# Kernel tuning notes

Hardware: AMD Instinct MI355X
Metric: run time of the kernel (lower is better)

## Reference

```python
import jax, jax.numpy as jnp
import numpy as np

KERNEL_SIZE = 5
SIGMA = 1.0
CHANNELS = 13
MAX_LEVELS = 3


def gaussian_kernel(size=KERNEL_SIZE, channels=CHANNELS, sigma=SIGMA):
    ax = np.linspace(-(size - 1) / 2.0, (size - 1) / 2.0, size)
    xx, yy = np.meshgrid(ax, ax)
    k = np.exp(-0.5 * (np.square(xx) + np.square(yy)) / np.square(sigma))
    k /= np.sum(k)
    # depthwise OIHW: (channels, 1, kh, kw), same kernel per channel
    return jnp.asarray(np.tile(k[None, None], (channels, 1, 1, 1)), dtype=jnp.float32)


def depthwise_gauss(x, kernel):
    c = kernel.shape[0]
    pad = kernel.shape[-1] // 2
    return jax.lax.conv_general_dilated(
        x, kernel, window_strides=(1, 1),
        padding=[(pad, pad), (pad, pad)],
        dimension_numbers=('NCHW', 'OIHW', 'NCHW'),
        feature_group_count=c)


def downsample(x):
    return x[:, :, ::2, ::2]


def upsample_nearest2x(x):
    return jnp.repeat(jnp.repeat(x, 2, axis=2), 2, axis=3)


def create_laplacian_pyramid(x, kernel, levels):
    pyramids = []
    cur = x
    for _ in range(levels):
        down = downsample(depthwise_gauss(cur, kernel))
        pyramids.append(cur - upsample_nearest2x(down))
        cur = down
    pyramids.append(cur)
    return pyramids


def setup_inputs() -> dict:
    key = jax.random.key(0)
    k1, k2 = jax.random.split(key)
    B, C, H, W = 16, CHANNELS, 512, 512
    x = jax.random.normal(k1, (B, C, H, W), dtype=jnp.float32)
    target = jax.random.normal(k2, (B, C, H, W), dtype=jnp.float32)
    kernel = gaussian_kernel()  # deterministic buffer, matches torch module
    return {"x": x, "target": target, "kernel": kernel}


def reference(x, target, kernel):
    x = x.astype(jnp.float32)
    target = target.astype(jnp.float32)
    px = create_laplacian_pyramid(x, kernel, MAX_LEVELS)
    pt = create_laplacian_pyramid(target, kernel, MAX_LEVELS)
    # torch F.l1_loss default reduction='mean' per level, summed over levels
    loss = jnp.asarray(0.0, dtype=jnp.float32)
    for a, b in zip(px, pt):
        loss = loss + jnp.mean(jnp.abs(a - b))
    return loss
```

## Files before the change

kernel.cpp:

```cpp
#include <hip/hip_runtime.h>


constexpr int THREADS = 256;
constexpr int TC = 32, TR = 16;
constexpr int ROWS = 2*TR + 3;
constexpr int COLS = 2*TC + 8;
constexpr int SEG4 = COLS/4;
constexpr int TOT4 = ROWS*SEG4;
constexpr int WOPS = (TOT4 + 63)/64;
constexpr int WREG = WOPS*64*4;
constexpr int HR = 11;

__device__ inline void gload_lds16(const float* g, float* l) {
    auto g1 = (const __attribute__((address_space(1))) void*)g;
    auto l3 = (__attribute__((address_space(3))) void*)l;
    __builtin_amdgcn_global_load_lds(g1, l3, 16, 0, 0);
}

template <int MW, bool FUSE, bool LAST, bool WRITE_DOWN>
__global__ __launch_bounds__(THREADS, MW)
void lap_level(const float* __restrict__ A,
               const float* __restrict__ Bp,
               const float* __restrict__ w25,
               float* __restrict__ down,
               float* __restrict__ P,
               int H, int W, int ntx, int nty, int ntiles, int level)
{
    __shared__ __align__(16) float sdA[2][WREG];
    __shared__ __align__(16) float sdB[2][FUSE ? WREG : 4];
    __shared__ float sdH[4][HR*TC];
    __shared__ float wsl[4], wsd[4];

    const int tid  = threadIdx.x;
    const int wv   = tid >> 6, lane = tid & 63;
    const int Hd = H >> 1, Wd = W >> 1;
    const int ntxy = ntx * nty;

    float g0, g1, g2, g3, g4;
    {
        float gg[5];
#pragma unroll
        for (int i = 0; i < 5; ++i) {
            float s = 0.f;
#pragma unroll
            for (int j = 0; j < 5; ++j) s += w25[i*5 + j];
            gg[i] = s;
        }
        g0 = gg[0]; g1 = gg[1]; g2 = gg[2]; g3 = gg[3]; g4 = gg[4];
    }

    float lsum = 0.f, dsum = 0.f;
    int cur = blockIdx.x;

    auto stage = [&](int t, int pp) {
        const int n   = t / ntxy;
        const int rem = t - n*ntxy;
        const int ty  = rem / ntx;
        const int tx  = rem - ty*ntx;
        const int gy0 = 2*ty*TR - 2;
        const int gx0 = 2*tx*TC - 4;
        const size_t ib = (size_t)n * H * W;
        for (int j = wv; j < WOPS; j += 4) {
            const int idx4 = j*64 + lane;
            const int r  = idx4 / SEG4;
            const int c4 = idx4 - r*SEG4;
            int gy = gy0 + r;          gy = gy < 0 ? 0 : (gy > H-1 ? H-1 : gy);
            int gx = gx0 + 4*c4;       gx = gx < 0 ? 0 : (gx > W-4 ? W-4 : gx);
            const size_t off = ib + (size_t)gy*W + gx;
            gload_lds16(A + off, &sdA[pp][j*256]);
            if (FUSE) gload_lds16(Bp + off, &sdB[pp][j*256]);
        }
    };

    auto compute = [&](int t, int pp) {
        const int n   = t / ntxy;
        const int rem = t - n*ntxy;
        const int ty  = rem / ntx;
        const int tx  = rem - ty*ntx;
        const float* ax = sdA[pp];
        const float* bx = FUSE ? sdB[pp] : sdA[pp];
        float* hh = sdH[wv];
        const int hb = 8*wv;
        const bool txL = (tx == 0), txR = (tx == ntx-1);

#pragma unroll
        for (int k = 0; k < (HR*TC + 63)/64; ++k) {
            const int idx = lane + 64*k;
            if (idx < HR*TC) {
                const int hr = idx >> 5, hc = idx & 31;
                const float gl0 = (txL & (hc == 0))  ? 0.f : g0;
                const float gl1 = (txL & (hc == 0))  ? 0.f : g1;
                const float gr4 = (txR & (hc == 31)) ? 0.f : g4;
                const float* pa = &ax[(hb+hr)*COLS + 2*hc + 2];
                float a0 = pa[0], a1 = pa[1], a2 = pa[2], a3 = pa[3], a4 = pa[4];
                if (FUSE) {
                    const float* pb = &bx[(hb+hr)*COLS + 2*hc + 2];
                    a0 -= pb[0]; a1 -= pb[1]; a2 -= pb[2]; a3 -= pb[3]; a4 -= pb[4];
                }
                float h = gl0*a0;
                h = fmaf(gl1, a1, h); h = fmaf(g2, a2, h);
                h = fmaf(g3, a3, h);  h = fmaf(gr4, a4, h);
                hh[hr*TC + hc] = h;
            }
        }
        const int ccx = lane & 31, rsub = lane >> 5;
#pragma unroll
        for (int q = 0; q < 2; ++q) {
            const int lr = rsub + 2*q;
            const bool mt = (ty == 0) & (wv == 0) & (lr == 0);
            const bool mb = (ty == nty-1) & (wv == 3) & (lr == 3);
            const float gv0 = mt ? 0.f : g0, gv1 = mt ? 0.f : g1;
            const float gv4 = mb ? 0.f : g4;
            float acc = gv0*hh[(2*lr)*TC + ccx];
            acc = fmaf(gv1, hh[(2*lr+1)*TC + ccx], acc);
            acc = fmaf(g2,  hh[(2*lr+2)*TC + ccx], acc);
            acc = fmaf(g3,  hh[(2*lr+3)*TC + ccx], acc);
            acc = fmaf(gv4, hh[(2*lr+4)*TC + ccx], acc);
            if (WRITE_DOWN) {
                const int gr = ty*TR + 4*wv + lr;
                down[(size_t)n*Hd*Wd + (size_t)gr*Wd + (tx*TC + ccx)] = acc;
            }
            const int cb = (hb + 2*lr + 2)*COLS + 2*ccx + 4;
            float c0 = ax[cb], c1 = ax[cb+1], c2 = ax[cb+COLS], c3 = ax[cb+COLS+1];
            if (FUSE) {
                c0 -= bx[cb];      c1 -= bx[cb+1];
                c2 -= bx[cb+COLS]; c3 -= bx[cb+COLS+1];
            }
            lsum += fabsf(c0-acc) + fabsf(c1-acc) + fabsf(c2-acc) + fabsf(c3-acc);
            if (LAST) dsum += fabsf(acc);
        }
    };

    if (cur < ntiles) {
        stage(cur, 0);
        int p = 0;
        for (;;) {
            asm volatile("s_waitcnt vmcnt(0)" ::: "memory");
            __builtin_amdgcn_s_barrier();
            __builtin_amdgcn_sched_barrier(0);

            const int nxt = cur + (int)gridDim.x;
            if (nxt < ntiles) stage(nxt, p ^ 1);
            __builtin_amdgcn_sched_barrier(0);

            compute(cur, p);

            if (nxt >= ntiles) break;
            cur = nxt; p ^= 1;
        }
    }

#pragma unroll
    for (int off = 32; off > 0; off >>= 1) {
        lsum += __shfl_down(lsum, off);
        if (LAST) dsum += __shfl_down(dsum, off);
    }
    __syncthreads();
    if (lane == 0) { wsl[wv] = lsum; if (LAST) wsd[wv] = dsum; }
    __syncthreads();
    if (tid == 0) {
        atomicAdd(&P[level*8 + (blockIdx.x & 7)], wsl[0]+wsl[1]+wsl[2]+wsl[3]);
        if (LAST)
            atomicAdd(&P[24 + (blockIdx.x & 7)], wsd[0]+wsd[1]+wsd[2]+wsd[3]);
    }
}

__global__ void finalize_kernel(const float* __restrict__ P,
                                float* __restrict__ out,
                                float inv0, float inv1, float inv2, float inv3)
{
    float s0 = 0.f, s1 = 0.f, s2 = 0.f, s3 = 0.f;
#pragma unroll
    for (int i = 0; i < 8; ++i) {
        s0 += P[i]; s1 += P[8+i]; s2 += P[16+i]; s3 += P[24+i];
    }
    out[0] = s0*inv0 + s1*inv1 + s2*inv2 + s3*inv3;
}

extern "C" void kernel_launch(void* const* d_in, const int* in_sizes, int n_in,
                              void* d_out, int out_size, void* d_ws, size_t ws_size,
                              hipStream_t stream)
{
    const float* x   = (const float*)d_in[0];
    const float* t   = (const float*)d_in[1];
    const float* ker = (const float*)d_in[2];
    float* out = (float*)d_out;

    constexpr int B = 16, C = 13, H = 512, W = 512;
    constexpr int N = B * C;

    float* P     = (float*)d_ws;
    float* down0 = (float*)((char*)d_ws + 256);
    float* down1 = down0 + (size_t)N * (H/2) * (W/2);

    hipMemsetAsync(P, 0, 32 * sizeof(float), stream);

    dim3 blk(THREADS);
    {
        const int ntx = (W/2)/TC, nty = (H/2)/TR;
        lap_level<3, true, false, true><<<dim3(768), blk, 0, stream>>>(
            x, t, ker, down0, P, H, W, ntx, nty, ntx*nty*N, 0);
    }
    {
        const int ntx = (W/4)/TC, nty = (H/4)/TR;
        lap_level<6, false, false, true><<<dim3(1536), blk, 0, stream>>>(
            down0, nullptr, ker, down1, P, H/2, W/2, ntx, nty, ntx*nty*N, 1);
    }
    {
        const int ntx = (W/8)/TC, nty = (H/8)/TR;
        lap_level<6, false, true, false><<<dim3(1536), blk, 0, stream>>>(
            down1, nullptr, ker, nullptr, P, H/4, W/4, ntx, nty, ntx*nty*N, 2);
    }

    const float inv0 = 1.0f / ((float)N * H * W);
    const float inv1 = 1.0f / ((float)N * (H/2) * (W/2));
    const float inv2 = 1.0f / ((float)N * (H/4) * (W/4));
    const float inv3 = 1.0f / ((float)N * (H/8) * (W/8));
    finalize_kernel<<<1, 1, 0, stream>>>(P, out, inv0, inv1, inv2, inv3);
}
```

Measured before the change: 211.5 us.

## Restructure pyramid levels into single-wave blocks with register-held horizontal pass

Replaces 256-thread blocks that worked on 32x16 output tiles with 64-thread single-wavefront blocks, each processing a contiguous run of 32x4 tiles that walk down columns so the vertical halo stays local. The horizontal blur now stays in registers instead of an LDS scratch buffer, and LDS reads use float2. Block barriers are replaced by counted vmcnt waits that let the next tile's async global-to-LDS load overlap the current compute. Smaller tiles mean a larger halo overhead (11 rows loaded per 8 used), and the grid and per-block tile counts are retuned for each level.

```diff
diff --git a/kernel.cpp b/kernel.cpp
--- a/kernel.cpp
+++ b/kernel.cpp
@@ -1,15 +1,12 @@
 #include <hip/hip_runtime.h>
 
 
-constexpr int THREADS = 256;
-constexpr int TC = 32, TR = 16;
-constexpr int ROWS = 2*TR + 3;
-constexpr int COLS = 2*TC + 8;
-constexpr int SEG4 = COLS/4;
-constexpr int TOT4 = ROWS*SEG4;
-constexpr int WOPS = (TOT4 + 63)/64;
-constexpr int WREG = WOPS*64*4;
-constexpr int HR = 11;
+constexpr int TPB   = 64;
+constexpr int SEG4  = 19;
+constexpr int STRIDE = 4 * SEG4;
+constexpr int SROWS = 11;
+constexpr int WOPS  = 4;
+constexpr int BUFSZ = WOPS * 64 * 4;
 
 __device__ inline void gload_lds16(const float* g, float* l) {
     auto g1 = (const __attribute__((address_space(1))) void*)g;
@@ -17,26 +14,24 @@
     __builtin_amdgcn_global_load_lds(g1, l3, 16, 0, 0);
 }
 
-template <int MW, bool FUSE, bool LAST, bool WRITE_DOWN>
-__global__ __launch_bounds__(THREADS, MW)
-void lap_level(const float* __restrict__ A,
-               const float* __restrict__ Bp,
-               const float* __restrict__ w25,
-               float* __restrict__ down,
-               float* __restrict__ P,
-               int H, int W, int ntx, int nty, int ntiles, int level)
+template <bool FUSE, bool LAST, bool WRITE_DOWN>
+__global__ __launch_bounds__(TPB)
+void lap_wave(const float* __restrict__ A,
+              const float* __restrict__ Bp,
+              const float* __restrict__ w25,
+              float* __restrict__ down,
+              float* __restrict__ P,
+              int H, int W, int ntx, int nty, int ntiles, int K, int level)
 {
-    __shared__ __align__(16) float sdA[2][WREG];
-    __shared__ __align__(16) float sdB[2][FUSE ? WREG : 4];
-    __shared__ float sdH[4][HR*TC];
-    __shared__ float wsl[4], wsd[4];
-
-    const int tid  = threadIdx.x;
-    const int wv   = tid >> 6, lane = tid & 63;
+    __shared__ __align__(16) float sA[2][BUFSZ];
+    __shared__ __align__(16) float sB[2][FUSE ? BUFSZ : 4];
+
+    const int lane = threadIdx.x;
+    const int c    = lane & 31;
+    const int rsub = lane >> 5;
     const int Hd = H >> 1, Wd = W >> 1;
-    const int ntxy = ntx * nty;
-
-    float g0, g1, g2, g3, g4;
+
+    float g0, g1v, g2, g3, g4;
     {
         float gg[5];
 #pragma unroll
@@ -46,107 +41,109 @@
             for (int j = 0; j < 5; ++j) s += w25[i*5 + j];
             gg[i] = s;
         }
-        g0 = gg[0]; g1 = gg[1]; g2 = gg[2]; g3 = gg[3]; g4 = gg[4];
-    }
+        g0 = gg[0]; g1v = gg[1]; g2 = gg[2]; g3 = gg[3]; g4 = gg[4];
+    }
+
+    int rc_[WOPS], cb_[WOPS];
+#pragma unroll
+    for (int j = 0; j < WOPS; ++j) {
+        const int idx = j*64 + lane;
+        const int r = idx / SEG4;
+        cb_[j] = 4 * (idx - r*SEG4);
+        rc_[j] = r > SROWS-1 ? SROWS-1 : r;
+    }
+
+    const int t0 = blockIdx.x * K;
+    const int t1 = (t0 + K < ntiles) ? (t0 + K) : ntiles;
 
     float lsum = 0.f, dsum = 0.f;
-    int cur = blockIdx.x;
-
-    auto stage = [&](int t, int pp) {
-        const int n   = t / ntxy;
-        const int rem = t - n*ntxy;
-        const int ty  = rem / ntx;
-        const int tx  = rem - ty*ntx;
-        const int gy0 = 2*ty*TR - 2;
-        const int gx0 = 2*tx*TC - 4;
-        const size_t ib = (size_t)n * H * W;
-        for (int j = wv; j < WOPS; j += 4) {
-            const int idx4 = j*64 + lane;
-            const int r  = idx4 / SEG4;
-            const int c4 = idx4 - r*SEG4;
-            int gy = gy0 + r;          gy = gy < 0 ? 0 : (gy > H-1 ? H-1 : gy);
-            int gx = gx0 + 4*c4;       gx = gx < 0 ? 0 : (gx > W-4 ? W-4 : gx);
-            const size_t off = ib + (size_t)gy*W + gx;
-            gload_lds16(A + off, &sdA[pp][j*256]);
-            if (FUSE) gload_lds16(Bp + off, &sdB[pp][j*256]);
-        }
-    };
-
-    auto compute = [&](int t, int pp) {
-        const int n   = t / ntxy;
-        const int rem = t - n*ntxy;
-        const int ty  = rem / ntx;
-        const int tx  = rem - ty*ntx;
-        const float* ax = sdA[pp];
-        const float* bx = FUSE ? sdB[pp] : sdA[pp];
-        float* hh = sdH[wv];
-        const int hb = 8*wv;
-        const bool txL = (tx == 0), txR = (tx == ntx-1);
-
-#pragma unroll
-        for (int k = 0; k < (HR*TC + 63)/64; ++k) {
-            const int idx = lane + 64*k;
-            if (idx < HR*TC) {
-                const int hr = idx >> 5, hc = idx & 31;
-                const float gl0 = (txL & (hc == 0))  ? 0.f : g0;
-                const float gl1 = (txL & (hc == 0))  ? 0.f : g1;
-                const float gr4 = (txR & (hc == 31)) ? 0.f : g4;
-                const float* pa = &ax[(hb+hr)*COLS + 2*hc + 2];
-                float a0 = pa[0], a1 = pa[1], a2 = pa[2], a3 = pa[3], a4 = pa[4];
-                if (FUSE) {
-                    const float* pb = &bx[(hb+hr)*COLS + 2*hc + 2];
-                    a0 -= pb[0]; a1 -= pb[1]; a2 -= pb[2]; a3 -= pb[3]; a4 -= pb[4];
+
+    if (t0 < t1) {
+        int cn, cx, cy;
+        { const int t = t0; cn = t/(ntx*nty);
+          const int r2 = t - cn*ntx*nty; cx = r2/nty; cy = r2 - cx*nty; }
+
+        auto stage = [&](int n, int sx, int ry, int pp) {
+            const int gy0 = 8*ry - 2;
+            const int gx0 = 64*sx - 4;
+            const size_t ib = (size_t)n * H * W;
+#pragma unroll
+            for (int j = 0; j < WOPS; ++j) {
+                int gy = gy0 + rc_[j]; gy = gy < 0 ? 0 : (gy > H-1 ? H-1 : gy);
+                int gx = gx0 + cb_[j]; gx = gx < 0 ? 0 : (gx > W-4 ? W-4 : gx);
+                const size_t off = ib + (size_t)gy*W + gx;
+                gload_lds16(A + off, &sA[pp][j*256]);
+                if constexpr (FUSE) gload_lds16(Bp + off, &sB[pp][j*256]);
+            }
+        };
+
+        auto compute = [&](int n, int sx, int ry, int pp) {
+            const float* ax = sA[pp];
+            const float* bx = FUSE ? sB[pp] : sA[pp];
+            const bool ec = (sx == 0) & (c == 0);
+            const float q0 = ec ? 0.f : g0, q1 = ec ? 0.f : g1v;
+            const float q4 = ((sx == ntx-1) & (c == 31)) ? 0.f : g4;
+            const int rb = 4*rsub;
+            float h[7];
+#pragma unroll
+            for (int s = 0; s < 7; ++s) {
+                const float* pa = &ax[(rb + s)*STRIDE + 2*c + 2];
+                const float2 A01 = *(const float2*)pa;
+                const float2 A23 = *(const float2*)(pa + 2);
+                const float2 A45 = *(const float2*)(pa + 4);
+                float a0 = A01.x, a1 = A01.y, a2 = A23.x, a3 = A23.y, a4 = A45.x;
+                if constexpr (FUSE) {
+                    const float* pb = &bx[(rb + s)*STRIDE + 2*c + 2];
+                    const float2 B01 = *(const float2*)pb;
+                    const float2 B23 = *(const float2*)(pb + 2);
+                    const float2 B45 = *(const float2*)(pb + 4);
+                    a0 -= B01.x; a1 -= B01.y; a2 -= B23.x; a3 -= B23.y; a4 -= B45.x;
                 }
-                float h = gl0*a0;
-                h = fmaf(gl1, a1, h); h = fmaf(g2, a2, h);
-                h = fmaf(g3, a3, h);  h = fmaf(gr4, a4, h);
-                hh[hr*TC + hc] = h;
-            }
-        }
-        const int ccx = lane & 31, rsub = lane >> 5;
-#pragma unroll
-        for (int q = 0; q < 2; ++q) {
-            const int lr = rsub + 2*q;
-            const bool mt = (ty == 0) & (wv == 0) & (lr == 0);
-            const bool mb = (ty == nty-1) & (wv == 3) & (lr == 3);
-            const float gv0 = mt ? 0.f : g0, gv1 = mt ? 0.f : g1;
-            const float gv4 = mb ? 0.f : g4;
-            float acc = gv0*hh[(2*lr)*TC + ccx];
-            acc = fmaf(gv1, hh[(2*lr+1)*TC + ccx], acc);
-            acc = fmaf(g2,  hh[(2*lr+2)*TC + ccx], acc);
-            acc = fmaf(g3,  hh[(2*lr+3)*TC + ccx], acc);
-            acc = fmaf(gv4, hh[(2*lr+4)*TC + ccx], acc);
-            if (WRITE_DOWN) {
-                const int gr = ty*TR + 4*wv + lr;
-                down[(size_t)n*Hd*Wd + (size_t)gr*Wd + (tx*TC + ccx)] = acc;
-            }
-            const int cb = (hb + 2*lr + 2)*COLS + 2*ccx + 4;
-            float c0 = ax[cb], c1 = ax[cb+1], c2 = ax[cb+COLS], c3 = ax[cb+COLS+1];
-            if (FUSE) {
-                c0 -= bx[cb];      c1 -= bx[cb+1];
-                c2 -= bx[cb+COLS]; c3 -= bx[cb+COLS+1];
-            }
-            lsum += fabsf(c0-acc) + fabsf(c1-acc) + fabsf(c2-acc) + fabsf(c3-acc);
-            if (LAST) dsum += fabsf(acc);
-        }
-    };
-
-    if (cur < ntiles) {
-        stage(cur, 0);
-        int p = 0;
-        for (;;) {
-            asm volatile("s_waitcnt vmcnt(0)" ::: "memory");
-            __builtin_amdgcn_s_barrier();
-            __builtin_amdgcn_sched_barrier(0);
-
-            const int nxt = cur + (int)gridDim.x;
-            if (nxt < ntiles) stage(nxt, p ^ 1);
-            __builtin_amdgcn_sched_barrier(0);
-
-            compute(cur, p);
-
-            if (nxt >= ntiles) break;
-            cur = nxt; p ^= 1;
+                h[s] = fmaf(q4, a4, fmaf(g3, a3, fmaf(g2, a2, fmaf(q1, a1, q0*a0))));
+            }
+#pragma unroll
+            for (int q = 0; q < 2; ++q) {
+                const int r  = 2*rsub + q;
+                const int gr = 4*ry + r;
+                const float v0 = (gr == 0) ? 0.f : g0;
+                const float v1 = (gr == 0) ? 0.f : g1v;
+                const float v4 = (gr == Hd-1) ? 0.f : g4;
+                const float acc =
+                    fmaf(v4, h[2*q+4], fmaf(g3, h[2*q+3],
+                    fmaf(g2, h[2*q+2], fmaf(v1, h[2*q+1], v0*h[2*q]))));
+                if constexpr (WRITE_DOWN)
+                    down[(size_t)n*Hd*Wd + (size_t)gr*Wd + (sx*32 + c)] = acc;
+                const int sr = (rb + 2*q + 2)*STRIDE + 2*c + 4;
+                const float2 X0 = *(const float2*)&ax[sr];
+                const float2 X1 = *(const float2*)&ax[sr + STRIDE];
+                float c0 = X0.x, c1 = X0.y, c2 = X1.x, c3 = X1.y;
+                if constexpr (FUSE) {
+                    const float2 Y0 = *(const float2*)&bx[sr];
+                    const float2 Y1 = *(const float2*)&bx[sr + STRIDE];
+                    c0 -= Y0.x; c1 -= Y0.y; c2 -= Y1.x; c3 -= Y1.y;
+                }
+                lsum += fabsf(c0 - acc) + fabsf(c1 - acc)
+                      + fabsf(c2 - acc) + fabsf(c3 - acc);
+                if constexpr (LAST) dsum += fabsf(acc);
+            }
+        };
+
+        stage(cn, cx, cy, 0);
+        int pp = 0;
+        for (int t = t0; t < t1; ++t) {
+            int nn = cn, nx = cx, ny = cy + 1;
+            if (ny == nty) { ny = 0; ++nx; if (nx == ntx) { nx = 0; ++nn; } }
+            if (t + 1 < t1) {
+                stage(nn, nx, ny, pp ^ 1);
+                if constexpr (FUSE)
+                    asm volatile("s_waitcnt vmcnt(8)" ::: "memory");
+                else
+                    asm volatile("s_waitcnt vmcnt(4)" ::: "memory");
+            } else {
+                asm volatile("s_waitcnt vmcnt(0)" ::: "memory");
+            }
+            compute(cn, cx, cy, pp);
+            cn = nn; cx = nx; cy = ny; pp ^= 1;
         }
     }
 
@@ -155,13 +152,9 @@
         lsum += __shfl_down(lsum, off);
         if (LAST) dsum += __shfl_down(dsum, off);
     }
-    __syncthreads();
-    if (lane == 0) { wsl[wv] = lsum; if (LAST) wsd[wv] = dsum; }
-    __syncthreads();
-    if (tid == 0) {
-        atomicAdd(&P[level*8 + (blockIdx.x & 7)], wsl[0]+wsl[1]+wsl[2]+wsl[3]);
-        if (LAST)
-            atomicAdd(&P[24 + (blockIdx.x & 7)], wsd[0]+wsd[1]+wsd[2]+wsd[3]);
+    if (lane == 0) {
+        atomicAdd(&P[level*8 + (blockIdx.x & 7)], lsum);
+        if (LAST) atomicAdd(&P[24 + (blockIdx.x & 7)], dsum);
     }
 }
 
@@ -195,21 +188,23 @@
 
     hipMemsetAsync(P, 0, 32 * sizeof(float), stream);
 
-    dim3 blk(THREADS);
-    {
-        const int ntx = (W/2)/TC, nty = (H/2)/TR;
-        lap_level<3, true, false, true><<<dim3(768), blk, 0, stream>>>(
-            x, t, ker, down0, P, H, W, ntx, nty, ntx*nty*N, 0);
-    }
-    {
-        const int ntx = (W/4)/TC, nty = (H/4)/TR;
-        lap_level<6, false, false, true><<<dim3(1536), blk, 0, stream>>>(
-            down0, nullptr, ker, down1, P, H/2, W/2, ntx, nty, ntx*nty*N, 1);
-    }
-    {
-        const int ntx = (W/8)/TC, nty = (H/8)/TR;
-        lap_level<6, false, true, false><<<dim3(1536), blk, 0, stream>>>(
-            down1, nullptr, ker, nullptr, P, H/4, W/4, ntx, nty, ntx*nty*N, 2);
+    {
+        const int ntx = (W/2)/32, nty = (H/2)/4, nt = ntx*nty*N;
+        const int grid = 2560, K = (nt + grid - 1)/grid;
+        lap_wave<true, false, true><<<grid, TPB, 0, stream>>>(
+            x, t, ker, down0, P, H, W, ntx, nty, nt, K, 0);
+    }
+    {
+        const int ntx = (W/4)/32, nty = (H/4)/4, nt = ntx*nty*N;
+        const int grid = 4096, K = (nt + grid - 1)/grid;
+        lap_wave<false, false, true><<<grid, TPB, 0, stream>>>(
+            down0, nullptr, ker, down1, P, H/2, W/2, ntx, nty, nt, K, 1);
+    }
+    {
+        const int ntx = (W/8)/32, nty = (H/8)/4, nt = ntx*nty*N;
+        const int grid = 2048, K = (nt + grid - 1)/grid;
+        lap_wave<false, true, false><<<grid, TPB, 0, stream>>>(
+            down1, nullptr, ker, nullptr, P, H/4, W/4, ntx, nty, nt, K, 2);
     }
 
     const float inv0 = 1.0f / ((float)N * H * W);
```

Result: slower. 325.0 us (+53.6%).

## Triple-buffer tile staging with contiguous per-block tile ranges and partial waits

Applied to the files above, without the earlier changes.

Replaces the double-buffered grid-stride loop with a three-stage LDS ring. Each block now walks a contiguous range of K tiles in column-major tile order and prefetches two tiles ahead, waiting with partial vmcnt counts instead of draining all loads. Load addresses are precomputed per thread, and grid sizes and occupancy hints are lowered to fit the larger LDS footprint. The aim is to hide more global-memory latency and improve locality between neighbouring tiles, at the cost of fewer resident blocks and hard-coded wait counts tied to the per-wave load count.

```diff
diff --git a/kernel.cpp b/kernel.cpp
--- a/kernel.cpp
+++ b/kernel.cpp
@@ -6,10 +6,10 @@
 constexpr int ROWS = 2*TR + 3;
 constexpr int COLS = 2*TC + 8;
 constexpr int SEG4 = COLS/4;
-constexpr int TOT4 = ROWS*SEG4;
-constexpr int WOPS = (TOT4 + 63)/64;
-constexpr int WREG = WOPS*64*4;
-constexpr int HR = 11;
+constexpr int OPS  = 12;
+constexpr int OPW  = OPS/4;
+constexpr int BUFF = OPS*64*4;
+constexpr int HR   = 11;
 
 __device__ inline void gload_lds16(const float* g, float* l) {
     auto g1 = (const __attribute__((address_space(1))) void*)g;
@@ -24,19 +24,19 @@
                const float* __restrict__ w25,
                float* __restrict__ down,
                float* __restrict__ P,
-               int H, int W, int ntx, int nty, int ntiles, int level)
+               int H, int W, int ntx, int nty, int ntiles, int K, int level)
 {
-    __shared__ __align__(16) float sdA[2][WREG];
-    __shared__ __align__(16) float sdB[2][FUSE ? WREG : 4];
+    __shared__ __align__(16) float sA[3][BUFF];
+    __shared__ __align__(16) float sB[3][FUSE ? BUFF : 4];
     __shared__ float sdH[4][HR*TC];
     __shared__ float wsl[4], wsd[4];
 
-    const int tid  = threadIdx.x;
-    const int wv   = tid >> 6, lane = tid & 63;
+    const int tid = threadIdx.x;
+    const int wv = tid >> 6, lane = tid & 63;
     const int Hd = H >> 1, Wd = W >> 1;
     const int ntxy = ntx * nty;
 
-    float g0, g1, g2, g3, g4;
+    float g0, g1v, g2, g3, g4;
     {
         float gg[5];
 #pragma unroll
@@ -46,39 +46,46 @@
             for (int j = 0; j < 5; ++j) s += w25[i*5 + j];
             gg[i] = s;
         }
-        g0 = gg[0]; g1 = gg[1]; g2 = gg[2]; g3 = gg[3]; g4 = gg[4];
-    }
-
+        g0 = gg[0]; g1v = gg[1]; g2 = gg[2]; g3 = gg[3]; g4 = gg[4];
+    }
+
+    int ru[OPW], cu[OPW], lo[OPW];
+#pragma unroll
+    for (int u = 0; u < OPW; ++u) {
+        const int j = wv*OPW + u;
+        const int idx4 = j*64 + lane;
+        const int r = idx4 / SEG4;
+        cu[u] = 4*(idx4 - r*SEG4);
+        ru[u] = r > ROWS-1 ? ROWS-1 : r;
+        lo[u] = j*256;
+    }
+
+    const int t0 = blockIdx.x * K;
+    const int t1 = (t0 + K < ntiles) ? t0 + K : ntiles;
     float lsum = 0.f, dsum = 0.f;
-    int cur = blockIdx.x;
 
     auto stage = [&](int t, int pp) {
-        const int n   = t / ntxy;
+        const int n  = t / ntxy;
         const int rem = t - n*ntxy;
-        const int ty  = rem / ntx;
-        const int tx  = rem - ty*ntx;
-        const int gy0 = 2*ty*TR - 2;
-        const int gx0 = 2*tx*TC - 4;
+        const int tx = rem / nty, ty = rem - (rem/nty)*nty;
+        const int gy0 = 2*ty*TR - 2, gx0 = 2*tx*TC - 4;
         const size_t ib = (size_t)n * H * W;
-        for (int j = wv; j < WOPS; j += 4) {
-            const int idx4 = j*64 + lane;
-            const int r  = idx4 / SEG4;
-            const int c4 = idx4 - r*SEG4;
-            int gy = gy0 + r;          gy = gy < 0 ? 0 : (gy > H-1 ? H-1 : gy);
-            int gx = gx0 + 4*c4;       gx = gx < 0 ? 0 : (gx > W-4 ? W-4 : gx);
+#pragma unroll
+        for (int u = 0; u < OPW; ++u) {
+            int gy = gy0 + ru[u]; gy = gy < 0 ? 0 : (gy > H-1 ? H-1 : gy);
+            int gx = gx0 + cu[u]; gx = gx < 0 ? 0 : (gx > W-4 ? W-4 : gx);
             const size_t off = ib + (size_t)gy*W + gx;
-            gload_lds16(A + off, &sdA[pp][j*256]);
-            if (FUSE) gload_lds16(Bp + off, &sdB[pp][j*256]);
+            gload_lds16(A + off, &sA[pp][lo[u]]);
+            if constexpr (FUSE) gload_lds16(Bp + off, &sB[pp][lo[u]]);
         }
     };
 
     auto compute = [&](int t, int pp) {
-        const int n   = t / ntxy;
+        const int n  = t / ntxy;
         const int rem = t - n*ntxy;
-        const int ty  = rem / ntx;
-        const int tx  = rem - ty*ntx;
-        const float* ax = sdA[pp];
-        const float* bx = FUSE ? sdB[pp] : sdA[pp];
+        const int tx = rem / nty, ty = rem - (rem/nty)*nty;
+        const float* ax = sA[pp];
+        const float* bx = FUSE ? sB[pp] : sA[pp];
         float* hh = sdH[wv];
         const int hb = 8*wv;
         const bool txL = (tx == 0), txR = (tx == ntx-1);
@@ -89,11 +96,11 @@
             if (idx < HR*TC) {
                 const int hr = idx >> 5, hc = idx & 31;
                 const float gl0 = (txL & (hc == 0))  ? 0.f : g0;
-                const float gl1 = (txL & (hc == 0))  ? 0.f : g1;
+                const float gl1 = (txL & (hc == 0))  ? 0.f : g1v;
                 const float gr4 = (txR & (hc == 31)) ? 0.f : g4;
                 const float* pa = &ax[(hb+hr)*COLS + 2*hc + 2];
                 float a0 = pa[0], a1 = pa[1], a2 = pa[2], a3 = pa[3], a4 = pa[4];
-                if (FUSE) {
+                if constexpr (FUSE) {
                     const float* pb = &bx[(hb+hr)*COLS + 2*hc + 2];
                     a0 -= pb[0]; a1 -= pb[1]; a2 -= pb[2]; a3 -= pb[3]; a4 -= pb[4];
                 }
@@ -109,44 +116,50 @@
             const int lr = rsub + 2*q;
             const bool mt = (ty == 0) & (wv == 0) & (lr == 0);
             const bool mb = (ty == nty-1) & (wv == 3) & (lr == 3);
-            const float gv0 = mt ? 0.f : g0, gv1 = mt ? 0.f : g1;
-            const float gv4 = mb ? 0.f : g4;
-            float acc = gv0*hh[(2*lr)*TC + ccx];
-            acc = fmaf(gv1, hh[(2*lr+1)*TC + ccx], acc);
-            acc = fmaf(g2,  hh[(2*lr+2)*TC + ccx], acc);
-            acc = fmaf(g3,  hh[(2*lr+3)*TC + ccx], acc);
-            acc = fmaf(gv4, hh[(2*lr+4)*TC + ccx], acc);
-            if (WRITE_DOWN) {
+            const float v0 = mt ? 0.f : g0, v1 = mt ? 0.f : g1v;
+            const float v4 = mb ? 0.f : g4;
+            float acc = v0*hh[(2*lr)*TC + ccx];
+            acc = fmaf(v1, hh[(2*lr+1)*TC + ccx], acc);
+            acc = fmaf(g2, hh[(2*lr+2)*TC + ccx], acc);
+            acc = fmaf(g3, hh[(2*lr+3)*TC + ccx], acc);
+            acc = fmaf(v4, hh[(2*lr+4)*TC + ccx], acc);
+            if constexpr (WRITE_DOWN) {
                 const int gr = ty*TR + 4*wv + lr;
                 down[(size_t)n*Hd*Wd + (size_t)gr*Wd + (tx*TC + ccx)] = acc;
             }
             const int cb = (hb + 2*lr + 2)*COLS + 2*ccx + 4;
             float c0 = ax[cb], c1 = ax[cb+1], c2 = ax[cb+COLS], c3 = ax[cb+COLS+1];
-            if (FUSE) {
+            if constexpr (FUSE) {
                 c0 -= bx[cb];      c1 -= bx[cb+1];
                 c2 -= bx[cb+COLS]; c3 -= bx[cb+COLS+1];
             }
             lsum += fabsf(c0-acc) + fabsf(c1-acc) + fabsf(c2-acc) + fabsf(c3-acc);
-            if (LAST) dsum += fabsf(acc);
+            if constexpr (LAST) dsum += fabsf(acc);
         }
     };
 
-    if (cur < ntiles) {
-        stage(cur, 0);
-        int p = 0;
-        for (;;) {
-            asm volatile("s_waitcnt vmcnt(0)" ::: "memory");
+    if (t0 < t1) {
+        stage(t0, 0);
+        if (t0 + 1 < t1) stage(t0 + 1, 1);
+        int pc = 0, ps = 2;
+        for (int t = t0; t < t1; ++t) {
             __builtin_amdgcn_s_barrier();
+            if (t + 2 < t1) stage(t + 2, ps);
+            const int ahead = (t1-1-t) < 2 ? (t1-1-t) : 2;
+            if constexpr (FUSE) {
+                if (ahead == 2)      asm volatile("s_waitcnt vmcnt(12)" ::: "memory");
+                else if (ahead == 1) asm volatile("s_waitcnt vmcnt(6)"  ::: "memory");
+                else                 asm volatile("s_waitcnt vmcnt(0)"  ::: "memory");
+            } else {
+                if (ahead == 2)      asm volatile("s_waitcnt vmcnt(6)"  ::: "memory");
+                else if (ahead == 1) asm volatile("s_waitcnt vmcnt(3)"  ::: "memory");
+                else                 asm volatile("s_waitcnt vmcnt(0)"  ::: "memory");
+            }
             __builtin_amdgcn_sched_barrier(0);
-
-            const int nxt = cur + (int)gridDim.x;
-            if (nxt < ntiles) stage(nxt, p ^ 1);
-            __builtin_amdgcn_sched_barrier(0);
-
-            compute(cur, p);
-
-            if (nxt >= ntiles) break;
-            cur = nxt; p ^= 1;
+            __builtin_amdgcn_s_barrier();
+            compute(t, pc);
+            pc = pc == 2 ? 0 : pc + 1;
+            ps = ps == 2 ? 0 : ps + 1;
         }
     }
 
@@ -198,18 +211,24 @@
     dim3 blk(THREADS);
     {
         const int ntx = (W/2)/TC, nty = (H/2)/TR;
-        lap_level<3, true, false, true><<<dim3(768), blk, 0, stream>>>(
-            x, t, ker, down0, P, H, W, ntx, nty, ntx*nty*N, 0);
+        const int nt = ntx*nty*N;
+        const int grid = 512, K = (nt + grid - 1)/grid;
+        lap_level<2, true, false, true><<<grid, blk, 0, stream>>>(
+            x, t, ker, down0, P, H, W, ntx, nty, nt, K, 0);
     }
     {
         const int ntx = (W/4)/TC, nty = (H/4)/TR;
-        lap_level<6, false, false, true><<<dim3(1536), blk, 0, stream>>>(
-            down0, nullptr, ker, down1, P, H/2, W/2, ntx, nty, ntx*nty*N, 1);
+        const int nt = ntx*nty*N;
+        const int grid = 768, K = (nt + grid - 1)/grid;
+        lap_level<3, false, false, true><<<grid, blk, 0, stream>>>(
+            down0, nullptr, ker, down1, P, H/2, W/2, ntx, nty, nt, K, 1);
     }
     {
         const int ntx = (W/8)/TC, nty = (H/8)/TR;
-        lap_level<6, false, true, false><<<dim3(1536), blk, 0, stream>>>(
-            down1, nullptr, ker, nullptr, P, H/4, W/4, ntx, nty, ntx*nty*N, 2);
+        const int nt = ntx*nty*N;
+        const int grid = 768, K = (nt + grid - 1)/grid;
+        lap_level<3, false, true, false><<<grid, blk, 0, stream>>>(
+            down1, nullptr, ker, nullptr, P, H/4, W/4, ntx, nty, nt, K, 2);
     }
 
     const float inv0 = 1.0f / ((float)N * H * W);
```

Result: slower. 221.9 us (+4.9%).
